# Kernel tuning notes

Hardware: AMD Instinct MI355X
Metric: run time of the kernel (lower is better)

## Reference

```python
import jax, jax.numpy as jnp
import numpy as np

# irreps_node_input = 64x0e + 16x1e  -> 64 scalars + 16 vectors (dim 112)
N_S = 64      # scalar channels
N_V = 16      # vector channels
H = 8         # attention heads
RBF = 128     # radial basis size
MID = 64      # radial MLP hidden
NW = N_S * 2 + N_V * 3   # 176 TP path weights per edge
ALPHA_C = (N_S + N_V) // H   # 80 scalars -> 10 per head
VEC_C = (N_S + N_V + N_V) // H  # 96 vec channels -> 12 per head


def _smooth_leaky(x, a=0.2):
    # SmoothLeakyReLU: x * (a + (1-a)*sigmoid(x))
    return x * (a + (1.0 - a) * jax.nn.sigmoid(x))


def _ln(x, eps=1e-5):
    m = jnp.mean(x, axis=-1, keepdims=True)
    v = jnp.var(x, axis=-1, keepdims=True)
    return (x - m) * jax.lax.rsqrt(v + eps)


def setup_inputs() -> dict:
    N, E = 50000, 400000
    key = jax.random.key(0)
    ks = jax.random.split(key, 16)
    D = N_S + 3 * N_V
    inp = {}
    inp['node_input'] = jax.random.normal(ks[0], (N, D), dtype=jnp.float32)
    inp['edge_src'] = jax.random.randint(ks[1], (E,), 0, N)
    inp['edge_dst'] = jax.random.randint(ks[2], (E,), 0, N)
    inp['edge_attr'] = jax.random.normal(ks[3], (E, 4), dtype=jnp.float32)      # sh: 1x0e+1x1e
    inp['edge_scalars'] = jax.random.normal(ks[4], (E, RBF), dtype=jnp.float32)  # RBF features
    # per-irrep linear weights (LinearRS style, 1/sqrt(fan_in) scale)
    inp['w_src_s'] = jax.random.normal(ks[5], (N_S, N_S), dtype=jnp.float32) / np.sqrt(N_S)
    inp['w_src_v'] = jax.random.normal(ks[6], (N_V, N_V), dtype=jnp.float32) / np.sqrt(N_V)
    inp['w_dst_s'] = jax.random.normal(ks[7], (N_S, N_S), dtype=jnp.float32) / np.sqrt(N_S)
    inp['w_dst_v'] = jax.random.normal(ks[8], (N_V, N_V), dtype=jnp.float32) / np.sqrt(N_V)
    # RadialProfile MLP
    inp['rad_w1'] = jax.random.normal(ks[9], (RBF, MID), dtype=jnp.float32) / np.sqrt(RBF)
    inp['rad_b1'] = jnp.zeros((MID,), dtype=jnp.float32)
    inp['rad_w2'] = jax.random.normal(ks[10], (MID, NW), dtype=jnp.float32) / np.sqrt(MID)
    inp['rad_b2'] = jnp.zeros((NW,), dtype=jnp.float32)
    # per-head alpha dot vector
    inp['alpha_dot'] = jax.random.normal(ks[11], (H, ALPHA_C), dtype=jnp.float32) / np.sqrt(ALPHA_C)
    # output projection (per-irrep)
    inp['proj_ws'] = jax.random.normal(ks[12], (N_S + N_V, N_S), dtype=jnp.float32) / np.sqrt(N_S + N_V)
    inp['proj_bs'] = jnp.zeros((N_S,), dtype=jnp.float32)
    inp['proj_wv'] = jax.random.normal(ks[13], (N_S + 2 * N_V, N_V), dtype=jnp.float32) / np.sqrt(N_S + 2 * N_V)
    return inp


def reference(node_input, edge_attr, edge_scalars, w_src_s, w_src_v, w_dst_s, w_dst_v,
              rad_w1, rad_b1, rad_w2, rad_b2, alpha_dot, proj_ws, proj_bs, proj_wv,
              edge_src, edge_dst):
    N = node_input.shape[0]
    E = edge_src.shape[0]
    s_in = node_input[:, :N_S]                              # [N, 64]
    v_in = node_input[:, N_S:].reshape(N, N_V, 3)           # [N, 16, 3]
    # merge_src / merge_dst equivariant linears, then gather onto edges
    s = (s_in @ w_src_s)[edge_src] + (s_in @ w_dst_s)[edge_dst]                    # [E, 64]
    v = jnp.einsum('ncd,ce->ned', v_in, w_src_v)[edge_src] \
        + jnp.einsum('ncd,ce->ned', v_in, w_dst_v)[edge_dst]                       # [E, 16, 3]
    e0 = edge_attr[:, 0]                                     # [E] 0e sh
    e1 = edge_attr[:, 1:4]                                   # [E, 3] 1e sh
    # RadialProfile: per-edge TP weights
    h = jax.nn.silu(_ln(edge_scalars @ rad_w1 + rad_b1))
    w = h @ rad_w2 + rad_b2                                  # [E, 176]
    w0 = w[:, :N_S]                  # 0e x 0e -> 0e
    w1 = w[:, N_S:2 * N_S]           # 0e x 1e -> 1e
    w2 = w[:, 2 * N_S:2 * N_S + N_V]             # 1e x 0e -> 1e
    w3 = w[:, 2 * N_S + N_V:2 * N_S + 2 * N_V]   # 1e x 1e -> 0e
    w4 = w[:, 2 * N_S + 2 * N_V:]                # 1e x 1e -> 1e
    inv_s3 = 1.0 / np.sqrt(3.0)
    inv_s2 = 1.0 / np.sqrt(2.0)
    # depthwise (uvu) tensor product, outputs sorted even-first: [64x0e, 16x0e, 64x1e, 16x1e, 16x1e]
    out_s = jnp.concatenate([
        w0 * s * e0[:, None],
        w3 * jnp.einsum('ekd,ed->ek', v, e1) * inv_s3,
    ], axis=1)                                               # [E, 80]
    out_v = jnp.concatenate([
        (w1 * s)[:, :, None] * e1[:, None, :],
        w2[:, :, None] * v * e0[:, None, None],
        w4[:, :, None] * jnp.cross(v, e1[:, None, :]) * inv_s2,
    ], axis=1)                                               # [E, 96, 3]
    # heads
    a_feat = out_s.reshape(E, H, ALPHA_C)                    # [E, 8, 10]
    alpha = jnp.einsum('ehc,hc->eh', _smooth_leaky(a_feat), alpha_dot)  # [E, 8]
    # segment softmax over destination nodes
    amax = jax.ops.segment_max(alpha, edge_dst, num_segments=N)
    amax = jnp.where(jnp.isfinite(amax), amax, 0.0)
    ex = jnp.exp(alpha - amax[edge_dst])
    den = jax.ops.segment_sum(ex, edge_dst, num_segments=N)
    attn = ex / (den[edge_dst] + 1e-9)                       # [E, 8]
    # values per head: scalars + flattened vector channels
    value = jnp.concatenate([a_feat, out_v.reshape(E, H, VEC_C * 3)], axis=2)  # [E, 8, 46]
    agg = jax.ops.segment_sum(attn[:, :, None] * value, edge_dst, num_segments=N)  # [N, 8, 46]
    s_agg = agg[:, :, :ALPHA_C].reshape(N, H * ALPHA_C)      # [N, 80]
    v_agg = agg[:, :, ALPHA_C:].reshape(N, H * VEC_C, 3)     # [N, 96, 3]
    # output projection (per-irrep linear with bias on scalars)
    out_sf = s_agg @ proj_ws + proj_bs                       # [N, 64]
    out_vf = jnp.einsum('ncd,ce->ned', v_agg, proj_wv).reshape(N, N_V * 3)  # [N, 48]
    return jnp.concatenate([out_sf, out_vf], axis=1)         # [N, 112]
```

## Files before the change

kernel.cpp:

```cpp
#include <hip/hip_runtime.h>
#include <hip/hip_bf16.h>

#define WST 184
#define CROW 264

typedef __attribute__((ext_vector_type(8))) short bf16x8;
typedef __attribute__((ext_vector_type(4))) float f32x4;

__device__ inline ushort f2bf(float f){
  union { __hip_bfloat16 b; ushort u; } v;
  v.b = __float2bfloat16(f);
  return v.u;
}
__device__ inline ushort f2h(float f){ _Float16 h=(_Float16)f; ushort u; __builtin_memcpy(&u,&h,2); return u; }
__device__ inline float h2f(ushort u){ _Float16 h; __builtin_memcpy(&h,&u,2); return (float)h; }

__global__ __launch_bounds__(256) void k_node(
  const float* __restrict__ ni,
  const float* __restrict__ wss, const float* __restrict__ wsv,
  const float* __restrict__ wds, const float* __restrict__ wdv,
  float* __restrict__ xs_s, float* __restrict__ xs_d,
  float* __restrict__ xv_s, float* __restrict__ xv_d, int N)
{
  __shared__ float sW0[64*64], sW1[64*64];
  __shared__ float sV0[256], sV1[256];
  __shared__ float sRow[4][112];
  int t = threadIdx.x, wid = t>>6, lane = t&63;
  for(int i=t;i<4096;i+=256){ sW0[i]=wss[i]; sW1[i]=wds[i]; }
  if(t<256){ sV0[t]=wsv[t]; sV1[t]=wdv[t]; }
  __syncthreads();
  for(int itn=0; itn<16; ++itn){
    int node = blockIdx.x*64 + itn*4 + wid;
    if(node>=N) continue;
    const float* row = ni + (size_t)node*112;
    if(lane<56) ((float2*)sRow[wid])[lane] = ((const float2*)row)[lane];
    float* r = sRow[wid];
    float a0=0.f, a1=0.f;
    #pragma unroll 8
    for(int k=0;k<64;k++){ float x=r[k]; a0+=x*sW0[k*64+lane]; a1+=x*sW1[k*64+lane]; }
    xs_s[(size_t)node*64+lane]=a0; xs_d[(size_t)node*64+lane]=a1;
    if(lane<48){
      int e_=lane/3, d_=lane-e_*3; float b0=0.f, b1=0.f;
      #pragma unroll
      for(int c=0;c<16;c++){ float x=r[64+c*3+d_]; b0+=x*sV0[c*16+e_]; b1+=x*sV1[c*16+e_]; }
      xv_s[(size_t)node*48+lane]=b0; xv_d[(size_t)node*48+lane]=b1;
    }
  }
}

__global__ void k_deg(const int* __restrict__ edst, int* __restrict__ deg, int E){
  int e = blockIdx.x*256 + threadIdx.x;
  if(e<E) atomicAdd(&deg[edst[e]], 1);
}

__global__ __launch_bounds__(256) void k_scan1(
  const int* __restrict__ deg, int* __restrict__ cur, int* __restrict__ bsum, int N)
{
  __shared__ int sb[256];
  int t = threadIdx.x, i = blockIdx.x*256 + t;
  int x = (i<N) ? deg[i] : 0;
  sb[t]=x; __syncthreads();
  int v=x;
  #pragma unroll
  for(int o=1;o<256;o<<=1){
    int u=(t>=o)?sb[t-o]:0; __syncthreads();
    v+=u; sb[t]=v; __syncthreads();
  }
  if(i<N) cur[i]=v-x;
  if(t==255) bsum[blockIdx.x]=v;
}

__global__ __launch_bounds__(256) void k_scan2(
  int* __restrict__ bsum, int* __restrict__ offs, int N, int nb)
{
  __shared__ int sb[256];
  int t = threadIdx.x;
  int x = (t<nb) ? bsum[t] : 0;
  sb[t]=x; __syncthreads();
  int v=x;
  #pragma unroll
  for(int o=1;o<256;o<<=1){
    int u=(t>=o)?sb[t-o]:0; __syncthreads();
    v+=u; sb[t]=v; __syncthreads();
  }
  if(t<nb) bsum[t]=v-x;
  if(t==nb-1) offs[N]=v;
}

__global__ void k_scan3(const int* __restrict__ bsum,
                        int* __restrict__ offs, int* __restrict__ cur, int N)
{
  int i = blockIdx.x*256 + threadIdx.x;
  if(i<N){ int v = cur[i] + bsum[blockIdx.x]; offs[i]=v; cur[i]=v; }
}

__global__ void k_fill(const int* __restrict__ esrc, const int* __restrict__ edst,
                       const float* __restrict__ eattr, int* __restrict__ cur,
                       int* __restrict__ pos_of, int* __restrict__ srcC,
                       int* __restrict__ dstC, float4* __restrict__ eaC, int E){
  int e = blockIdx.x*256 + threadIdx.x;
  if(e<E){
    int p = atomicAdd(&cur[edst[e]], 1);
    pos_of[e] = p;
    srcC[p] = esrc[e];
    dstC[p] = edst[e];
    eaC[p] = *(const float4*)&eattr[(size_t)e*4];
  }
}

__global__ __launch_bounds__(256) void k_mlp(
  const float* __restrict__ escal,
  const float* __restrict__ w1, const float* __restrict__ b1,
  const float* __restrict__ w2, const float* __restrict__ b2,
  const int* __restrict__ pos_of,
  _Float16* __restrict__ wbuf, int E)
{
  __shared__ __align__(16) ushort sW1t[64*136];
  __shared__ __align__(16) ushort sW2t[176*72];
  __shared__ __align__(16) ushort ubuf[4][16*WST];
  int t = threadIdx.x, wid = t>>6, lane = t&63;
  int r16 = lane&15, g = lane>>4;

  for(int i=t;i<128*64;i+=256){ int k=i>>6, n=i&63; sW1t[n*136+k]=f2bf(w1[i]); }
  for(int i=t;i<64*176;i+=256){ int k=i/176, n=i-k*176; sW2t[n*72+k]=f2bf(w2[i]); }
  __syncthreads();

  float b1v[4], b2v[11];
  #pragma unroll
  for(int nt=0;nt<4;nt++) b1v[nt]=b1[nt*16+r16];
  #pragma unroll
  for(int s=0;s<11;s++) b2v[s]=b2[s*16+r16];

  ushort* ub = ubuf[wid];
  _Float16* wsb = (_Float16*)ub;

  int ntiles = (E+15)>>4;
  int nw = gridDim.x*4;

  for(int wt = blockIdx.x*4+wid; wt < ntiles; wt += nw){
    int ebase = wt*16;
    int erow = ebase + r16; if(erow >= E) erow = E-1;

    f32x4 acc[4];
    #pragma unroll
    for(int nt=0;nt<4;nt++) acc[nt]=(f32x4){0,0,0,0};
    #pragma unroll
    for(int ks=0;ks<4;ks++){
      const float* p = escal + (size_t)erow*128 + ks*32 + g*8;
      float4 va = *(const float4*)p;
      float4 vb = *(const float4*)(p+4);
      bf16x8 af;
      af[0]=(short)f2bf(va.x); af[1]=(short)f2bf(va.y);
      af[2]=(short)f2bf(va.z); af[3]=(short)f2bf(va.w);
      af[4]=(short)f2bf(vb.x); af[5]=(short)f2bf(vb.y);
      af[6]=(short)f2bf(vb.z); af[7]=(short)f2bf(vb.w);
      #pragma unroll
      for(int nt=0;nt<4;nt++){
        bf16x8 bf = *(const bf16x8*)&sW1t[(nt*16+r16)*136 + ks*32 + g*8];
        acc[nt] = __builtin_amdgcn_mfma_f32_16x16x32_bf16(af,bf,acc[nt],0,0,0);
      }
    }

    #pragma unroll
    for(int nt=0;nt<4;nt++)
      #pragma unroll
      for(int q=0;q<4;q++) acc[nt][q] += b1v[nt];
    #pragma unroll
    for(int q=0;q<4;q++){
      float s = acc[0][q]+acc[1][q]+acc[2][q]+acc[3][q];
      float ss = acc[0][q]*acc[0][q]+acc[1][q]*acc[1][q]+acc[2][q]*acc[2][q]+acc[3][q]*acc[3][q];
      #pragma unroll
      for(int o=1;o<16;o<<=1){ s += __shfl_xor(s,o); ss += __shfl_xor(ss,o); }
      float m = s*(1.f/64.f);
      float var = ss*(1.f/64.f) - m*m;
      float inv = rsqrtf(var + 1e-5f);
      int rr = g*4+q;
      #pragma unroll
      for(int nt=0;nt<4;nt++){
        float xn = (acc[nt][q]-m)*inv;
        float h = xn/(1.f+__expf(-xn));
        ub[rr*72 + nt*16 + r16] = f2bf(h);
      }
    }

    bf16x8 af2[2];
    af2[0] = *(const bf16x8*)&ub[r16*72 + 0*32 + g*8];
    af2[1] = *(const bf16x8*)&ub[r16*72 + 1*32 + g*8];
    f32x4 c2[11];
    #pragma unroll
    for(int s=0;s<11;s++) c2[s]=(f32x4){0,0,0,0};
    #pragma unroll
    for(int ks=0;ks<2;ks++){
      #pragma unroll
      for(int s=0;s<11;s++){
        bf16x8 bf = *(const bf16x8*)&sW2t[(s*16+r16)*72 + ks*32 + g*8];
        c2[s] = __builtin_amdgcn_mfma_f32_16x16x32_bf16(af2[ks],bf,c2[s],0,0,0);
      }
    }
    #pragma unroll
    for(int s=0;s<11;s++){
      int col = s*16 + r16;
      #pragma unroll
      for(int q=0;q<4;q++){
        wsb[(g*4+q)*WST + col] = (_Float16)(c2[s][q] + b2v[s]);
      }
    }
    int pv = 0;
    if(lane<16 && ebase+lane < E) pv = pos_of[ebase+lane];
    int rows = E - ebase; if(rows > 16) rows = 16;
    const float4* srcv = (const float4*)ub;
    int tot4 = rows*23;
    for(int i=lane; i<tot4; i+=64){
      int r = i/23, c = i - 23*r;
      int pos = __shfl(pv, r);
      ((float4*)(wbuf + (size_t)pos*WST))[c] = srcv[i];
    }
  }
}

__global__ __launch_bounds__(256) void k_geo(
  const int* __restrict__ srcC, const int* __restrict__ dstC,
  const float4* __restrict__ eaC, const _Float16* __restrict__ wbuf,
  const float* __restrict__ adot,
  const float* __restrict__ xs_s, const float* __restrict__ xs_d,
  const float* __restrict__ xv_s, const float* __restrict__ xv_d,
  _Float16* __restrict__ cbuf, float* __restrict__ alphaC, int E)
{
  __shared__ float sAdot[80];
  __shared__ float sP[4][80];
  int t = threadIdx.x, wid = t>>6, lane = t&63;
  if(t<80) sAdot[t]=adot[t];
  __syncthreads();

  float* P = sP[wid];
  int nw = gridDim.x*4;
  const float inv_s3 = 0.5773502691896258f, inv_s2 = 0.7071067811865475f;

  int l3 = lane/3;
  int d  = lane - l3*3;
  int k3 = l3*3;
  int d1 = (d==2)?0:d+1;
  int d2 = (d==0)?2:d-1;
  int l3c = l3&15;
  int sA = (lane*3)&63, sB = (lane*3+1)&63, sC = (lane*3+2)&63;
  int cs1 = (k3+d1)&63, cs2 = (k3+d2)&63;
  int hh5 = (lane>>1)&7, st5 = hh5*10 + (lane&1)*5;
  float adl = sAdot[lane];
  float ad2 = sAdot[64+(lane&15)];

  for(int p = blockIdx.x*4+wid; p < E; p += nw){
    int si = srcC[p], di = dstC[p];
    float4 ea = eaC[p];
    const _Float16* wr = wbuf + (size_t)p*WST;
    float S = xs_s[(size_t)si*64+lane] + xs_d[(size_t)di*64+lane];
    float Vl = (lane<48) ? (xv_s[(size_t)si*48+lane] + xv_d[(size_t)di*48+lane]) : 0.f;
    float w0 = (float)wr[lane];
    float w1v = (float)wr[64+lane];
    float sc = w0*S*ea.x;
    float sg = 1.f/(1.f+__expf(-sc));
    P[lane] = sc*(0.2f + 0.8f*sg)*adl;
    float v0=__shfl(Vl,sA), v1=__shfl(Vl,sB), v2=__shfl(Vl,sC);
    float vd3 = v0*ea.y + v1*ea.z + v2*ea.w;
    float sc2 = (float)wr[144+(lane&15)]*vd3*inv_s3;
    if(lane<16){
      float sg2 = 1.f/(1.f+__expf(-sc2));
      P[64+lane] = sc2*(0.2f + 0.8f*sg2)*ad2;
    }
    float s5 = P[st5] + P[st5+1] + P[st5+2] + P[st5+3] + P[st5+4];
    float aL = __shfl(s5, 2*(lane&7)) + __shfl(s5, 2*(lane&7)+1);
    if(lane<8) alphaC[(size_t)p*8+lane] = aL;
    float scBv = __shfl(sc2, lane&15);
    float Vd1 = __shfl(Vl, cs1), Vd2 = __shfl(Vl, cs2);
    float wslot = scBv;
    if(lane<48){
      float e1d1 = (d1==0)?ea.y:((d1==1)?ea.z:ea.w);
      float e1d2 = (d2==0)?ea.y:((d2==1)?ea.z:ea.w);
      float cr = Vd1*e1d2 - Vd2*e1d1;
      wslot = (float)wr[160+l3c]*cr*inv_s2;
    }
    float w2v_pre = (lane<48) ? (float)wr[128+l3c]*ea.x*Vl : 0.f;
    ushort4 ck;
    ck.x = f2h(w1v*S);
    ck.y = f2h(w2v_pre);
    ck.z = f2h(sc);
    ck.w = f2h(wslot);
    _Float16* cr_ = cbuf + (size_t)p*CROW;
    *(ushort4*)(cr_ + (size_t)lane*4) = ck;
    if(lane==0) *(float4*)((char*)cr_ + 512) = ea;
  }
}

#define EDGE_PROC(b, ck_, ea_, w1x,w1y,w1z,sc,aa,xx) { \
  const float* ar_ = alphaC + (size_t)(b)*8; \
  float evW1_ = ar_[hW1], evSC_ = ar_[hSC], evA_ = ar_[hA], evX_ = ar_[hX]; \
  float ws1_ = h2f(ck_.x), scA_ = h2f(ck_.z), wv_ = h2f(ck_.w); \
  float vA_ = (lane<48) ? h2f(ck_.y) : wv_; \
  float t1_ = evW1_*ws1_; \
  w1x += t1_*ea_.y; w1y += t1_*ea_.z; w1z += t1_*ea_.w; \
  sc += evSC_*scA_; aa += evA_*vA_; xx += evX_*wv_; }

__global__ __launch_bounds__(256) void k_agg(
  const int* __restrict__ offs, float* __restrict__ alphaC,
  const _Float16* __restrict__ cbuf,
  const float* __restrict__ pws, const float* __restrict__ pbs,
  const float* __restrict__ pwv, float* __restrict__ out, int N)
{
  __shared__ float sVa[4][288];
  __shared__ float sSa[4][80];
  int t=threadIdx.x, wid=t>>6, lane=t&63;

  float* Va = sVa[wid];
  float* Sa = sSa[wid];

  int l3 = lane/3;
  int d  = lane - l3*3;
  int hW1 = lane/12;
  int hX  = (80+l3)/12;
  int hSC = lane/10;
  int hA  = (lane<48) ? (64+l3)/12 : (64+(lane-48))/10;
  int h8 = lane&7;

  int nw4 = gridDim.x*4;
  for(int n = blockIdx.x*4+wid; n < N; n += nw4){
    int s0 = offs[n], s1 = offs[n+1];

    float mx = -1e30f;
    for(int b = s0 + (lane>>3); b < s1; b += 8)
      mx = fmaxf(mx, alphaC[(size_t)b*8 + h8]);
    mx = fmaxf(mx, __shfl_xor(mx, 8));
    mx = fmaxf(mx, __shfl_xor(mx, 16));
    mx = fmaxf(mx, __shfl_xor(mx, 32));

    float dn = 0.f;
    for(int b = s0 + (lane>>3); b < s1; b += 8){
      size_t ix = (size_t)b*8 + h8;
      float ev = __expf(alphaC[ix] - mx);
      alphaC[ix] = ev;
      dn += ev;
    }
    dn += __shfl_xor(dn, 8);
    dn += __shfl_xor(dn, 16);
    dn += __shfl_xor(dn, 32);
    float rdn = 1.0f/(dn + 1e-9f);
    float rW1 = __shfl(rdn, hW1);
    float rSC = __shfl(rdn, hSC);
    float rA  = __shfl(rdn, hA);
    float rX  = __shfl(rdn, hX);

    float w1xA=0.f,w1yA=0.f,w1zA=0.f,scAc=0.f,aaA=0.f,xxA=0.f;
    float w1xB=0.f,w1yB=0.f,w1zB=0.f,scBc=0.f,aaB=0.f,xxB=0.f;
    int b = s0;
    for(; b+3 < s1; b += 4){
      const _Float16* c0 = cbuf + (size_t)(b  )*CROW;
      const _Float16* c1 = cbuf + (size_t)(b+1)*CROW;
      const _Float16* c2 = cbuf + (size_t)(b+2)*CROW;
      const _Float16* c3 = cbuf + (size_t)(b+3)*CROW;
      ushort4 k0 = *(const ushort4*)(c0 + (size_t)lane*4);
      ushort4 k1 = *(const ushort4*)(c1 + (size_t)lane*4);
      ushort4 k2 = *(const ushort4*)(c2 + (size_t)lane*4);
      ushort4 k3v= *(const ushort4*)(c3 + (size_t)lane*4);
      float4 e0 = *(const float4*)((const char*)c0 + 512);
      float4 e1 = *(const float4*)((const char*)c1 + 512);
      float4 e2 = *(const float4*)((const char*)c2 + 512);
      float4 e3 = *(const float4*)((const char*)c3 + 512);
      EDGE_PROC(b,   k0, e0, w1xA,w1yA,w1zA,scAc,aaA,xxA)
      EDGE_PROC(b+1, k1, e1, w1xB,w1yB,w1zB,scBc,aaB,xxB)
      EDGE_PROC(b+2, k2, e2, w1xA,w1yA,w1zA,scAc,aaA,xxA)
      EDGE_PROC(b+3, k3v,e3, w1xB,w1yB,w1zB,scBc,aaB,xxB)
    }
    for(; b < s1; ++b){
      const _Float16* c0 = cbuf + (size_t)b*CROW;
      ushort4 k0 = *(const ushort4*)(c0 + (size_t)lane*4);
      float4 e0 = *(const float4*)((const char*)c0 + 512);
      EDGE_PROC(b, k0, e0, w1xA,w1yA,w1zA,scAc,aaA,xxA)
    }
    float w1x=w1xA+w1xB, w1y=w1yA+w1yB, w1z=w1zA+w1zB;
    float sc=scAc+scBc, aa=aaA+aaB, xx=xxA+xxB;

    Va[lane*3+0] = w1x*rW1;
    Va[lane*3+1] = w1y*rW1;
    Va[lane*3+2] = w1z*rW1;
    if(lane<48){
      Va[192+lane] = aa*rA;
      Va[240+lane] = xx*rX;
    } else {
      Sa[64+(lane-48)] = aa*rA;
    }
    Sa[lane] = sc*rSC;

    float o1 = pbs[lane];
    #pragma unroll 8
    for(int i=0;i<80;i++) o1 += Sa[i]*pws[i*64+lane];
    out[(size_t)n*112+lane] = o1;
    if(lane<48){
      float o2 = 0.f;
      #pragma unroll 8
      for(int k=0;k<64;k++) o2 += Va[k*3+d]*pwv[k*16+l3];
      #pragma unroll
      for(int k=0;k<16;k++) o2 += Va[192+k*3+d]*pwv[(64+k)*16+l3];
      #pragma unroll
      for(int k=0;k<16;k++) o2 += Va[240+k*3+d]*pwv[(80+k)*16+l3];
      out[(size_t)n*112+64+lane] = o2;
    }
  }
}

extern "C" void kernel_launch(void* const* d_in, const int* in_sizes, int n_in,
                              void* d_out, int out_size, void* d_ws, size_t ws_size,
                              hipStream_t stream)
{
  const int N = in_sizes[0]/112;
  const int E = in_sizes[1];
  const float* ni    = (const float*)d_in[0];
  const int*   esrc  = (const int*)d_in[1];
  const int*   edst  = (const int*)d_in[2];
  const float* eattr = (const float*)d_in[3];
  const float* escal = (const float*)d_in[4];
  const float* wss   = (const float*)d_in[5];
  const float* wsv   = (const float*)d_in[6];
  const float* wds   = (const float*)d_in[7];
  const float* wdv   = (const float*)d_in[8];
  const float* rw1   = (const float*)d_in[9];
  const float* rb1   = (const float*)d_in[10];
  const float* rw2   = (const float*)d_in[11];
  const float* rb2   = (const float*)d_in[12];
  const float* adot  = (const float*)d_in[13];
  const float* pws   = (const float*)d_in[14];
  const float* pbs   = (const float*)d_in[15];
  const float* pwv   = (const float*)d_in[16];
  float* out = (float*)d_out;

  char* ws = (char*)d_ws;
  size_t off = 0;
  auto alloc = [&](size_t bytes)->void*{
    void* p = ws + off;
    off = (off + bytes + 255) & ~(size_t)255;
    return p;
  };
  float*    xs_s  = (float*)   alloc((size_t)N*64*4);
  float*    xs_d  = (float*)   alloc((size_t)N*64*4);
  float*    xv_s  = (float*)   alloc((size_t)N*48*4);
  float*    xv_d  = (float*)   alloc((size_t)N*48*4);
  _Float16* wbuf  = (_Float16*)alloc((size_t)E*WST*2);
  _Float16* cbuf  = (_Float16*)alloc((size_t)E*CROW*2);
  float*    alphaC= (float*)   alloc((size_t)E*8*4);
  int*      pos_of= (int*)     alloc((size_t)E*4);
  int*      srcC  = (int*)     alloc((size_t)E*4);
  int*      dstC  = (int*)     alloc((size_t)E*4);
  float4*   eaC   = (float4*)  alloc((size_t)E*16);
  int*      deg   = (int*)     alloc((size_t)N*4);
  int*      offs  = (int*)     alloc((size_t)(N+1)*4);
  int*      cur   = (int*)     alloc((size_t)N*4);
  int*      bsum  = (int*)     alloc(256*4);

  const int nb = (N+255)/256;

  hipMemsetAsync(deg, 0, (size_t)N*4, stream);

  k_node<<<(N+63)/64, 256, 0, stream>>>(ni, wss, wsv, wds, wdv, xs_s, xs_d, xv_s, xv_d, N);
  k_deg<<<(E+255)/256, 256, 0, stream>>>(edst, deg, E);
  k_scan1<<<nb, 256, 0, stream>>>(deg, cur, bsum, N);
  k_scan2<<<1, 256, 0, stream>>>(bsum, offs, N, nb);
  k_scan3<<<nb, 256, 0, stream>>>(bsum, offs, cur, N);
  k_fill<<<(E+255)/256, 256, 0, stream>>>(esrc, edst, eattr, cur, pos_of, srcC, dstC, eaC, E);

  k_mlp<<<512, 256, 0, stream>>>(escal, rw1, rb1, rw2, rb2, pos_of, wbuf, E);

  k_geo<<<2048, 256, 0, stream>>>(srcC, dstC, eaC, wbuf, adot,
        xs_s, xs_d, xv_s, xv_d, cbuf, alphaC, E);

  k_agg<<<2048, 256, 0, stream>>>(offs, alphaC, cbuf, pws, pbs, pwv, out, N);
}
```

Baseline: 646.1 us.

## Split output projection into separate MFMA kernel fed by fp16 aggregate buffer

The per-node output projection is moved out of the aggregation kernel. k_agg now only writes the normalized aggregated features as fp16 rows (stride 384) to a workspace buffer. A new k_proj kernel loads 16-node tiles into shared memory and computes the scalar and vector projections with 16x16x32 fp16 MFMA instructions. The aim is to replace the scalar per-lane dot-product loops, which reloaded projection weights from global memory, with matrix-core work. This adds an extra global round trip through the fp16 buffer and an extra launch, and it lowers the precision of the aggregated values to fp16.

```diff
diff --git a/kernel.cpp b/kernel.cpp
--- a/kernel.cpp
+++ b/kernel.cpp
@@ -3,8 +3,10 @@
 
 #define WST 184
 #define CROW 264
+#define PST 384
 
 typedef __attribute__((ext_vector_type(8))) short bf16x8;
+typedef __attribute__((ext_vector_type(8))) _Float16 f16x8;
 typedef __attribute__((ext_vector_type(4))) float f32x4;
 
 __device__ inline ushort f2bf(float f){
@@ -302,18 +304,11 @@
 __global__ __launch_bounds__(256) void k_agg(
   const int* __restrict__ offs, float* __restrict__ alphaC,
   const _Float16* __restrict__ cbuf,
-  const float* __restrict__ pws, const float* __restrict__ pbs,
-  const float* __restrict__ pwv, float* __restrict__ out, int N)
-{
-  __shared__ float sVa[4][288];
-  __shared__ float sSa[4][80];
-  int t=threadIdx.x, wid=t>>6, lane=t&63;
-
-  float* Va = sVa[wid];
-  float* Sa = sSa[wid];
+  _Float16* __restrict__ aggH, int N)
+{
+  int wid=threadIdx.x>>6, lane=threadIdx.x&63;
 
   int l3 = lane/3;
-  int d  = lane - l3*3;
   int hW1 = lane/12;
   int hX  = (80+l3)/12;
   int hSC = lane/10;
@@ -377,30 +372,95 @@
     float w1x=w1xA+w1xB, w1y=w1yA+w1yB, w1z=w1zA+w1zB;
     float sc=scAc+scBc, aa=aaA+aaB, xx=xxA+xxB;
 
-    Va[lane*3+0] = w1x*rW1;
-    Va[lane*3+1] = w1y*rW1;
-    Va[lane*3+2] = w1z*rW1;
+    _Float16* ah = aggH + (size_t)n*PST;
+    ah[3*lane]   = (_Float16)(w1x*rW1);
+    ah[3*lane+1] = (_Float16)(w1y*rW1);
+    ah[3*lane+2] = (_Float16)(w1z*rW1);
     if(lane<48){
-      Va[192+lane] = aa*rA;
-      Va[240+lane] = xx*rX;
+      ah[192+lane] = (_Float16)(aa*rA);
+      ah[240+lane] = (_Float16)(xx*rX);
     } else {
-      Sa[64+(lane-48)] = aa*rA;
-    }
-    Sa[lane] = sc*rSC;
-
-    float o1 = pbs[lane];
-    #pragma unroll 8
-    for(int i=0;i<80;i++) o1 += Sa[i]*pws[i*64+lane];
-    out[(size_t)n*112+lane] = o1;
-    if(lane<48){
-      float o2 = 0.f;
-      #pragma unroll 8
-      for(int k=0;k<64;k++) o2 += Va[k*3+d]*pwv[k*16+l3];
-      #pragma unroll
-      for(int k=0;k<16;k++) o2 += Va[192+k*3+d]*pwv[(64+k)*16+l3];
-      #pragma unroll
-      for(int k=0;k<16;k++) o2 += Va[240+k*3+d]*pwv[(80+k)*16+l3];
-      out[(size_t)n*112+64+lane] = o2;
+      ah[352+(lane-48)] = (_Float16)(aa*rA);
+    }
+    ah[288+lane] = (_Float16)(sc*rSC);
+    if(lane<16) ah[368+lane] = (_Float16)0.f;
+  }
+}
+
+__global__ __launch_bounds__(256) void k_proj(
+  const _Float16* __restrict__ aggH,
+  const float* __restrict__ pws, const float* __restrict__ pbs,
+  const float* __restrict__ pwv, float* __restrict__ out, int N)
+{
+  __shared__ __align__(16) ushort sWsT[64*96];
+  __shared__ __align__(16) ushort sWvT[16*96];
+  __shared__ float sPb[64];
+  __shared__ __align__(16) ushort sA[4][16*PST];
+  int t = threadIdx.x, wid = t>>6, lane = t&63;
+  int r16 = lane&15, g = lane>>4;
+
+  for(int i=t;i<64*96;i+=256){ int j=i/96, k=i-96*j; sWsT[i] = (k<80)? f2h(pws[k*64+j]) : (ushort)0; }
+  for(int i=t;i<16*96;i+=256){ int e=i/96, k=i-96*e; sWvT[i] = f2h(pwv[k*16+e]); }
+  if(t<64) sPb[t]=pbs[t];
+  __syncthreads();
+
+  ushort* A = sA[wid];
+  int ntiles = (N+15)>>4;
+  int nw = gridDim.x*4;
+
+  for(int tile = blockIdx.x*4+wid; tile < ntiles; tile += nw){
+    int nb = tile*16;
+    for(int i=lane; i<16*48; i+=64){
+      int r = i>>5 ? i/48 : i/48;
+      r = i/48; int c = i - 48*r;
+      int row = nb + r; if(row >= N) row = N-1;
+      ((uint4*)&A[r*PST])[c] = ((const uint4*)(aggH + (size_t)row*PST))[c];
+    }
+
+    f32x4 acc[4];
+    #pragma unroll
+    for(int nt=0;nt<4;nt++) acc[nt]=(f32x4){0,0,0,0};
+    #pragma unroll
+    for(int ks=0;ks<3;ks++){
+      f16x8 af = *(const f16x8*)&A[r16*PST + 288 + ks*32 + g*8];
+      #pragma unroll
+      for(int nt=0;nt<4;nt++){
+        f16x8 bf = *(const f16x8*)&sWsT[(nt*16+r16)*96 + ks*32 + g*8];
+        acc[nt] = __builtin_amdgcn_mfma_f32_16x16x32_f16(af,bf,acc[nt],0,0,0);
+      }
+    }
+    #pragma unroll
+    for(int nt=0;nt<4;nt++){
+      int col = nt*16 + r16;
+      float bb = sPb[col];
+      #pragma unroll
+      for(int q=0;q<4;q++){
+        int node = nb + g*4 + q;
+        if(node < N) out[(size_t)node*112 + col] = acc[nt][q] + bb;
+      }
+    }
+
+    #pragma unroll
+    for(int rt=0;rt<3;rt++){
+      int r = rt*16 + r16;
+      int ln = r/3, dd = r - 3*ln;
+      f32x4 c2 = (f32x4){0,0,0,0};
+      #pragma unroll
+      for(int ks=0;ks<3;ks++){
+        int kbase = ks*32 + g*8;
+        f16x8 af;
+        #pragma unroll
+        for(int e=0;e<8;e++) af[e] = *(const _Float16*)&A[ln*PST + 3*(kbase+e) + dd];
+        f16x8 bf = *(const f16x8*)&sWvT[r16*96 + kbase];
+        c2 = __builtin_amdgcn_mfma_f32_16x16x32_f16(af,bf,c2,0,0,0);
+      }
+      #pragma unroll
+      for(int q=0;q<4;q++){
+        int pr = rt*16 + g*4 + q;
+        int lq = pr/3, dq = pr - 3*lq;
+        int node = nb + lq;
+        if(node < N) out[(size_t)node*112 + 64 + r16*3 + dq] = c2[q];
+      }
     }
   }
 }
@@ -443,6 +503,7 @@
   float*    xv_d  = (float*)   alloc((size_t)N*48*4);
   _Float16* wbuf  = (_Float16*)alloc((size_t)E*WST*2);
   _Float16* cbuf  = (_Float16*)alloc((size_t)E*CROW*2);
+  _Float16* aggH  = (_Float16*)alloc((size_t)N*PST*2);
   float*    alphaC= (float*)   alloc((size_t)E*8*4);
   int*      pos_of= (int*)     alloc((size_t)E*4);
   int*      srcC  = (int*)     alloc((size_t)E*4);
@@ -469,5 +530,7 @@
   k_geo<<<2048, 256, 0, stream>>>(srcC, dstC, eaC, wbuf, adot,
         xs_s, xs_d, xv_s, xv_d, cbuf, alphaC, E);
 
-  k_agg<<<2048, 256, 0, stream>>>(offs, alphaC, cbuf, pws, pbs, pwv, out, N);
-}
+  k_agg<<<4096, 256, 0, stream>>>(offs, alphaC, cbuf, aggH, N);
+
+  k_proj<<<512, 256, 0, stream>>>(aggH, pws, pbs, pwv, out, N);
+}
```

New measurement: 548.0 us. -15.2%, faster.
